# Optimization experiments

Measured on AMD Instinct MI355X. Metric: run time of the kernel, lower is better.

The kernel has to match this reference:

```python
import jax, jax.numpy as jnp
import numpy as np

HBLK = 16  # hadamard / nvfp4 block size
FP4_LEVELS = jnp.array([0.0, 0.5, 1.0, 1.5, 2.0, 3.0, 4.0, 6.0], dtype=jnp.float32)
FP4_MIDS = jnp.array([0.25, 0.75, 1.25, 1.75, 2.5, 3.5, 5.0], dtype=jnp.float32)


def _hadamard(n):
    H = np.array([[1.0]])
    while H.shape[0] < n:
        H = np.block([[H, H], [H, -H]])
    return jnp.asarray(H / np.sqrt(n), dtype=jnp.float32)  # orthonormal

H16 = _hadamard(HBLK)


def rht_forward(x, signs):
    # x: [M, K], K % 16 == 0 (no padding needed). Random sign diag then block Hadamard.
    M, K = x.shape
    xb = x.reshape(M, K // HBLK, HBLK)
    return ((xb * signs) @ H16).reshape(M, K)


def q_emulate(x):
    # NVFP4 quantize->dequantize along last dim: blocks of 16, E4M3 block scale = amax/6,
    # round-to-nearest onto E2M1 grid {0,.5,1,1.5,2,3,4,6} (signed).
    M, K = x.shape
    xb = x.reshape(M, K // HBLK, HBLK)
    amax = jnp.max(jnp.abs(xb), axis=-1, keepdims=True)
    scale = (amax / 6.0).astype(jnp.float8_e4m3fn).astype(x.dtype)
    safe = jnp.where(scale == 0, 1.0, scale)
    a = jnp.clip(jnp.abs(xb) / safe, 0.0, 6.0)
    q = FP4_LEVELS[jnp.searchsorted(FP4_MIDS, a)]
    return (jnp.sign(xb) * q * scale).reshape(M, K)


def setup_inputs() -> dict:
    key = jax.random.key(0)
    kx, kw, kb, ks1, ks2 = jax.random.split(key, 5)
    IN, OUT = 4096, 4096
    x = jax.random.normal(kx, (4, 2048, IN), dtype=jnp.float32)
    weight = jax.random.normal(kw, (OUT, IN), dtype=jnp.float32) / np.sqrt(IN)
    bound = 1.0 / np.sqrt(IN)
    bias = jax.random.uniform(kb, (OUT,), dtype=jnp.float32, minval=-bound, maxval=bound)
    signs_in = jnp.where(jax.random.bernoulli(ks1, 0.5, (HBLK,)), 1.0, -1.0).astype(jnp.float32)
    signs_grad = jnp.where(jax.random.bernoulli(ks2, 0.5, (HBLK,)), 1.0, -1.0).astype(jnp.float32)
    return {"x": x, "weight": weight, "bias": bias, "signs_in": signs_in, "signs_grad": signs_grad}


def reference(x, weight, bias, signs_in, signs_grad):
    # signs_grad only used in backward (kept for interface parity).
    x_flat = x.reshape(-1, x.shape[-1])
    x_q = q_emulate(rht_forward(x_flat, signs_in))
    w_q = q_emulate(rht_forward(weight, signs_in))
    y = x_q @ w_q.T + bias
    return y.reshape(*x.shape[:-1], weight.shape[0])
```

## Files before the change

kernel.cpp:

```cpp
#include <hip/hip_runtime.h>
#include <stdint.h>


typedef __bf16 bf16x8 __attribute__((ext_vector_type(8)));
typedef float f32x4 __attribute__((ext_vector_type(4)));


__device__ __forceinline__ float e4m3_rt(float x) {
    unsigned int u = __float_as_uint(x);
    int ex = (int)((u >> 23) & 0xffu) - 127;
    if (ex < -6) ex = -6;
    float qs = __uint_as_float((unsigned)(127 + 3 - ex) << 23);
    float qi = __uint_as_float((unsigned)(127 + ex - 3) << 23);
    return rintf(x * qs) * qi;
}

__global__ __launch_bounds__(256) void quant_rht_kernel(
    const float* __restrict__ X, const float* __restrict__ signs,
    uint16_t* __restrict__ Q, int ngroups)
{
    int gid = blockIdx.x * 256 + threadIdx.x;
    if (gid >= ngroups) return;

    const float4* p = (const float4*)(X + (size_t)gid * 16);
    float4 v0 = p[0], v1 = p[1], v2 = p[2], v3 = p[3];
    float t[16] = { v0.x, v0.y, v0.z, v0.w, v1.x, v1.y, v1.z, v1.w,
                    v2.x, v2.y, v2.z, v2.w, v3.x, v3.y, v3.z, v3.w };
#pragma unroll
    for (int i = 0; i < 16; i++) t[i] *= signs[i];

#pragma unroll
    for (int len = 1; len < 16; len <<= 1) {
#pragma unroll
        for (int i = 0; i < 16; i += 2 * len) {
#pragma unroll
            for (int j = 0; j < len; j++) {
                float a = t[i + j], b = t[i + j + len];
                t[i + j] = a + b;
                t[i + j + len] = a - b;
            }
        }
    }
    float amax = 0.0f;
#pragma unroll
    for (int i = 0; i < 16; i++) { t[i] *= 0.25f; amax = fmaxf(amax, fabsf(t[i])); }

    float scale = e4m3_rt(amax / 6.0f);
    float safe = (scale == 0.0f) ? 1.0f : scale;

    unsigned int w[8];
#pragma unroll
    for (int i = 0; i < 8; i++) {
        float d01[2];
#pragma unroll
        for (int h = 0; h < 2; h++) {
            float tv = t[2 * i + h];
            float aa = fminf(fabsf(tv) / safe, 6.0f);
            float q = aa > 2.5f ? (aa > 5.0f ? 6.0f : (aa > 3.5f ? 4.0f : 3.0f))
                                : (aa > 1.25f ? (aa > 1.75f ? 2.0f : 1.5f)
                                              : (aa > 0.75f ? 1.0f
                                                 : (aa > 0.25f ? 0.5f : 0.0f)));
            d01[h] = copysignf(q * scale, tv);
        }
        w[i] = (__float_as_uint(d01[0]) >> 16) |
               (__float_as_uint(d01[1]) & 0xFFFF0000u);
    }
    uint4* q4 = (uint4*)(Q + (size_t)gid * 16);
    q4[0] = make_uint4(w[0], w[1], w[2], w[3]);
    q4[1] = make_uint4(w[4], w[5], w[6], w[7]);
}


#define TM 128
#define TN 128
#define BK 64

__global__ __launch_bounds__(256) void gemm_bt_bias(
    const uint16_t* __restrict__ A,
    const uint16_t* __restrict__ B,
    const float* __restrict__ bias,
    float* __restrict__ C,
    int M, int N, int K)
{
    __shared__ uint4 As[TM * BK / 8];
    __shared__ uint4 Bs[TN * BK / 8];

    const int tid  = threadIdx.x;
    const int bm   = blockIdx.y, bn = blockIdx.x;
    const int wave = tid >> 6,  lane = tid & 63;
    const int wm   = wave >> 1, wn = wave & 1;
    const int lm   = lane & 15, g4 = lane >> 4;

    const int sr = tid >> 3;
    const int kg = (tid & 7) ^ (sr & 7);
    const uint16_t* ag = A + (size_t)(bm * TM + sr) * (size_t)K + kg * 8;
    const uint16_t* bg = B + (size_t)(bn * TN + sr) * (size_t)K + kg * 8;
    char* asd = (char*)&As[0] + tid * 16;
    char* bsd = (char*)&Bs[0] + tid * 16;

    f32x4 acc[4][4];
#pragma unroll
    for (int i = 0; i < 4; i++)
#pragma unroll
        for (int j = 0; j < 4; j++) acc[i][j] = (f32x4){0.f, 0.f, 0.f, 0.f};

    for (int kt = 0; kt < K; kt += BK) {
        __syncthreads();
#pragma unroll
        for (int i = 0; i < 4; i++) {
            __builtin_amdgcn_global_load_lds(
                (const __attribute__((address_space(1))) unsigned int*)(ag + (size_t)i * 32 * K),
                (__attribute__((address_space(3))) unsigned int*)(asd + i * 4096),
                16, 0, 0);
            __builtin_amdgcn_global_load_lds(
                (const __attribute__((address_space(1))) unsigned int*)(bg + (size_t)i * 32 * K),
                (__attribute__((address_space(3))) unsigned int*)(bsd + i * 4096),
                16, 0, 0);
        }
        ag += BK; bg += BK;
        __syncthreads();

#pragma unroll
        for (int ks = 0; ks < 2; ks++) {
            bf16x8 af[4], bf[4];
#pragma unroll
            for (int i = 0; i < 4; i++) {
                int rA = wm * 64 + i * 16 + lm;
                af[i] = __builtin_bit_cast(bf16x8, As[rA * 8 + ((ks * 4 + g4) ^ (lm & 7))]);
                int rB = wn * 64 + i * 16 + lm;
                bf[i] = __builtin_bit_cast(bf16x8, Bs[rB * 8 + ((ks * 4 + g4) ^ (lm & 7))]);
            }
#pragma unroll
            for (int i = 0; i < 4; i++)
#pragma unroll
                for (int j = 0; j < 4; j++)
                    acc[i][j] = __builtin_amdgcn_mfma_f32_16x16x32_bf16(
                        af[i], bf[j], acc[i][j], 0, 0, 0);
        }
    }

#pragma unroll
    for (int j = 0; j < 4; j++) {
        int col = bn * TN + wn * 64 + j * 16 + lm;
        float bj = bias[col];
#pragma unroll
        for (int i = 0; i < 4; i++) {
            int row0 = bm * TM + wm * 64 + i * 16 + g4 * 4;
#pragma unroll
            for (int r = 0; r < 4; r++) {
                C[(size_t)(row0 + r) * (size_t)N + col] = acc[i][j][r] + bj;
            }
        }
    }
}


extern "C" void kernel_launch(void* const* d_in, const int* in_sizes, int n_in,
                              void* d_out, int out_size, void* d_ws, size_t ws_size,
                              hipStream_t stream)
{
    const float* x        = (const float*)d_in[0];
    const float* w        = (const float*)d_in[1];
    const float* bias     = (const float*)d_in[2];
    const float* signs_in = (const float*)d_in[3];

    const int OUT = in_sizes[2];
    const int IN  = in_sizes[1] / OUT;
    const int M   = in_sizes[0] / IN;

    uint16_t* xq = (uint16_t*)d_ws;
    uint16_t* wq = xq + (size_t)M * (size_t)IN;
    (void)ws_size; (void)n_in; (void)out_size;

    int ngx = (int)((size_t)M * IN / 16);
    int ngw = (int)((size_t)OUT * IN / 16);
    quant_rht_kernel<<<(ngx + 255) / 256, 256, 0, stream>>>(x, signs_in, xq, ngx);
    quant_rht_kernel<<<(ngw + 255) / 256, 256, 0, stream>>>(w, signs_in, wq, ngw);

    dim3 grid(OUT / TN, M / TM);
    gemm_bt_bias<<<grid, 256, 0, stream>>>(xq, wq, bias, (float*)d_out, M, OUT, IN);
}
```

Baseline: 586.6 us.

## Rewrite GEMM as 256x256 multi-stage pipelined kernel and stage quant I/O via LDS

The GEMM moves from 128x128 tiles with 256 threads and a single LDS buffer to 256x256 tiles with 512 threads. It uses an 8-slot LDS ring of half-tiles filled by global_load_lds several stages ahead, with explicit vmcnt/lgkmcnt waits, barriers and setprio around the MFMA phases, so global loads overlap compute and reuse per tile increases. The quantize kernel now stages its input and output through swizzled shared memory so both reads and writes are coalesced. The bounds checks are dropped, so the code assumes the sizes divide evenly, and the deeper pipeline uses more LDS and registers.

```diff
diff --git a/kernel.cpp b/kernel.cpp
--- a/kernel.cpp
+++ b/kernel.cpp
@@ -19,15 +19,32 @@
     const float* __restrict__ X, const float* __restrict__ signs,
     uint16_t* __restrict__ Q, int ngroups)
 {
-    int gid = blockIdx.x * 256 + threadIdx.x;
-    if (gid >= ngroups) return;
-
-    const float4* p = (const float4*)(X + (size_t)gid * 16);
-    float4 v0 = p[0], v1 = p[1], v2 = p[2], v3 = p[3];
-    float t[16] = { v0.x, v0.y, v0.z, v0.w, v1.x, v1.y, v1.z, v1.w,
-                    v2.x, v2.y, v2.z, v2.w, v3.x, v3.y, v3.z, v3.w };
-#pragma unroll
-    for (int i = 0; i < 16; i++) t[i] *= signs[i];
+    (void)ngroups;
+    __shared__ uint4 sbuf[1024];
+    const int t = threadIdx.x;
+    const size_t gbase = (size_t)blockIdx.x * 256;
+
+    const uint4* src = (const uint4*)(X + gbase * 16);
+#pragma unroll
+    for (int it = 0; it < 4; ++it) {
+        int c = it * 256 + t;
+        sbuf[c ^ ((c >> 3) & 7)] = src[c];
+    }
+    __syncthreads();
+
+    float tv[16];
+#pragma unroll
+    for (int i = 0; i < 4; ++i) {
+        int c = 4 * t + i;
+        uint4 u = sbuf[c ^ ((c >> 3) & 7)];
+        tv[4 * i + 0] = __uint_as_float(u.x);
+        tv[4 * i + 1] = __uint_as_float(u.y);
+        tv[4 * i + 2] = __uint_as_float(u.z);
+        tv[4 * i + 3] = __uint_as_float(u.w);
+    }
+
+#pragma unroll
+    for (int i = 0; i < 16; i++) tv[i] *= signs[i];
 
 #pragma unroll
     for (int len = 1; len < 16; len <<= 1) {
@@ -35,15 +52,15 @@
         for (int i = 0; i < 16; i += 2 * len) {
 #pragma unroll
             for (int j = 0; j < len; j++) {
-                float a = t[i + j], b = t[i + j + len];
-                t[i + j] = a + b;
-                t[i + j + len] = a - b;
+                float a = tv[i + j], b = tv[i + j + len];
+                tv[i + j] = a + b;
+                tv[i + j + len] = a - b;
             }
         }
     }
     float amax = 0.0f;
 #pragma unroll
-    for (int i = 0; i < 16; i++) { t[i] *= 0.25f; amax = fmaxf(amax, fabsf(t[i])); }
+    for (int i = 0; i < 16; i++) { tv[i] *= 0.25f; amax = fmaxf(amax, fabsf(tv[i])); }
 
     float scale = e4m3_rt(amax / 6.0f);
     float safe = (scale == 0.0f) ? 1.0f : scale;
@@ -54,100 +71,159 @@
         float d01[2];
 #pragma unroll
         for (int h = 0; h < 2; h++) {
-            float tv = t[2 * i + h];
-            float aa = fminf(fabsf(tv) / safe, 6.0f);
+            float x = tv[2 * i + h];
+            float aa = fminf(fabsf(x) / safe, 6.0f);
             float q = aa > 2.5f ? (aa > 5.0f ? 6.0f : (aa > 3.5f ? 4.0f : 3.0f))
                                 : (aa > 1.25f ? (aa > 1.75f ? 2.0f : 1.5f)
                                               : (aa > 0.75f ? 1.0f
                                                  : (aa > 0.25f ? 0.5f : 0.0f)));
-            d01[h] = copysignf(q * scale, tv);
+            d01[h] = copysignf(q * scale, x);
         }
         w[i] = (__float_as_uint(d01[0]) >> 16) |
                (__float_as_uint(d01[1]) & 0xFFFF0000u);
     }
-    uint4* q4 = (uint4*)(Q + (size_t)gid * 16);
-    q4[0] = make_uint4(w[0], w[1], w[2], w[3]);
-    q4[1] = make_uint4(w[4], w[5], w[6], w[7]);
-}
-
-
-#define TM 128
-#define TN 128
-#define BK 64
-
-__global__ __launch_bounds__(256) void gemm_bt_bias(
+
+    __syncthreads();
+    {
+        int c0 = 2 * t, c1 = 2 * t + 1;
+        sbuf[c0 ^ ((c0 >> 3) & 7)] = make_uint4(w[0], w[1], w[2], w[3]);
+        sbuf[c1 ^ ((c1 >> 3) & 7)] = make_uint4(w[4], w[5], w[6], w[7]);
+    }
+    __syncthreads();
+
+    uint4* dst = (uint4*)(Q + gbase * 16);
+#pragma unroll
+    for (int it = 0; it < 2; ++it) {
+        int c = it * 256 + t;
+        dst[c] = sbuf[c ^ ((c >> 3) & 7)];
+    }
+}
+
+
+#define BM 256
+#define BN 256
+
+__global__ __launch_bounds__(512, 2) void gemm_bt_bias(
     const uint16_t* __restrict__ A,
     const uint16_t* __restrict__ B,
     const float* __restrict__ bias,
     float* __restrict__ C,
     int M, int N, int K)
 {
-    __shared__ uint4 As[TM * BK / 8];
-    __shared__ uint4 Bs[TN * BK / 8];
+    __shared__ uint4 sh[8][1024];
 
     const int tid  = threadIdx.x;
-    const int bm   = blockIdx.y, bn = blockIdx.x;
-    const int wave = tid >> 6,  lane = tid & 63;
-    const int wm   = wave >> 1, wn = wave & 1;
-    const int lm   = lane & 15, g4 = lane >> 4;
-
-    const int sr = tid >> 3;
-    const int kg = (tid & 7) ^ (sr & 7);
-    const uint16_t* ag = A + (size_t)(bm * TM + sr) * (size_t)K + kg * 8;
-    const uint16_t* bg = B + (size_t)(bn * TN + sr) * (size_t)K + kg * 8;
-    char* asd = (char*)&As[0] + tid * 16;
-    char* bsd = (char*)&Bs[0] + tid * 16;
-
-    f32x4 acc[4][4];
-#pragma unroll
-    for (int i = 0; i < 4; i++)
-#pragma unroll
-        for (int j = 0; j < 4; j++) acc[i][j] = (f32x4){0.f, 0.f, 0.f, 0.f};
-
-    for (int kt = 0; kt < K; kt += BK) {
-        __syncthreads();
-#pragma unroll
-        for (int i = 0; i < 4; i++) {
-            __builtin_amdgcn_global_load_lds(
-                (const __attribute__((address_space(1))) unsigned int*)(ag + (size_t)i * 32 * K),
-                (__attribute__((address_space(3))) unsigned int*)(asd + i * 4096),
-                16, 0, 0);
-            __builtin_amdgcn_global_load_lds(
-                (const __attribute__((address_space(1))) unsigned int*)(bg + (size_t)i * 32 * K),
-                (__attribute__((address_space(3))) unsigned int*)(bsd + i * 4096),
-                16, 0, 0);
-        }
-        ag += BK; bg += BK;
-        __syncthreads();
-
-#pragma unroll
-        for (int ks = 0; ks < 2; ks++) {
-            bf16x8 af[4], bf[4];
-#pragma unroll
-            for (int i = 0; i < 4; i++) {
-                int rA = wm * 64 + i * 16 + lm;
-                af[i] = __builtin_bit_cast(bf16x8, As[rA * 8 + ((ks * 4 + g4) ^ (lm & 7))]);
-                int rB = wn * 64 + i * 16 + lm;
-                bf[i] = __builtin_bit_cast(bf16x8, Bs[rB * 8 + ((ks * 4 + g4) ^ (lm & 7))]);
-            }
-#pragma unroll
-            for (int i = 0; i < 4; i++)
-#pragma unroll
-                for (int j = 0; j < 4; j++)
-                    acc[i][j] = __builtin_amdgcn_mfma_f32_16x16x32_bf16(
-                        af[i], bf[j], acc[i][j], 0, 0, 0);
-        }
-    }
-
-#pragma unroll
-    for (int j = 0; j < 4; j++) {
-        int col = bn * TN + wn * 64 + j * 16 + lm;
+    const int lane = tid & 63;
+    const int wave = tid >> 6;
+    const int wm = wave >> 2, wn = wave & 3;
+    const int lm = lane & 15, g4 = lane >> 4;
+    const int bn = blockIdx.x, bm = blockIdx.y;
+
+    const int NT  = K >> 6;
+    const int NHT = NT << 2;
+
+    const int p0 = tid, p1 = 512 + tid;
+    const int c0 = p0 ^ ((p0 >> 3) & 7);
+    const int c1 = p1 ^ ((p1 >> 3) & 7);
+    const uint16_t* asrc0 = A + (size_t)(bm * BM + (c0 >> 2)) * K + (c0 & 3) * 8;
+    const uint16_t* asrc1 = A + (size_t)(bm * BM + (c1 >> 2)) * K + (c1 & 3) * 8;
+    const uint16_t* bsrc0 = B + (size_t)(bn * BN + (c0 >> 2)) * K + (c0 & 3) * 8;
+    const uint16_t* bsrc1 = B + (size_t)(bn * BN + (c1 >> 2)) * K + (c1 & 3) * 8;
+    char* ldsd0 = (char*)&sh[0][0] + p0 * 16;
+    char* ldsd1 = (char*)&sh[0][0] + p1 * 16;
+
+    int aPos[8], bPos[4];
+#pragma unroll
+    for (int f = 0; f < 8; ++f) {
+        int c = (wm * 128 + f * 16 + lm) * 4 + g4;
+        aPos[f] = c ^ ((c >> 3) & 7);
+    }
+#pragma unroll
+    for (int f = 0; f < 4; ++f) {
+        int c = (wn * 64 + f * 16 + lm) * 4 + g4;
+        bPos[f] = c ^ ((c >> 3) & 7);
+    }
+
+    f32x4 acc[8][4];
+#pragma unroll
+    for (int i = 0; i < 8; ++i)
+#pragma unroll
+        for (int j = 0; j < 4; ++j) acc[i][j] = (f32x4){0.f, 0.f, 0.f, 0.f};
+    bf16x8 bfr[4];
+
+#define STAGE(jj) do {                                                        \
+    int _j = (jj);                                                            \
+    int _koff = (_j < NHT) ? (((_j >> 2) << 6) | (((_j >> 1) & 1) << 5)) : 0; \
+    int _sb = (_j & 7) << 14;                                                 \
+    const uint16_t* _s0 = (_j & 1) ? bsrc0 : asrc0;                           \
+    const uint16_t* _s1 = (_j & 1) ? bsrc1 : asrc1;                           \
+    __builtin_amdgcn_global_load_lds(                                         \
+        (const __attribute__((address_space(1))) unsigned int*)(_s0 + _koff), \
+        (__attribute__((address_space(3))) unsigned int*)(ldsd0 + _sb),       \
+        16, 0, 0);                                                            \
+    __builtin_amdgcn_global_load_lds(                                         \
+        (const __attribute__((address_space(1))) unsigned int*)(_s1 + _koff), \
+        (__attribute__((address_space(3))) unsigned int*)(ldsd1 + _sb),       \
+        16, 0, 0);                                                            \
+} while (0)
+
+#define PHASE(PAR, KS, RH, Q, GATE) do {                                      \
+    bf16x8 af_[4];                                                            \
+    _Pragma("unroll")                                                         \
+    for (int _i = 0; _i < 4; ++_i)                                            \
+        af_[_i] = __builtin_bit_cast(bf16x8,                                  \
+            sh[4*(PAR) + 2*(KS)][aPos[4*(RH) + _i]]);                         \
+    if ((Q) & 1) {                                                            \
+        _Pragma("unroll")                                                     \
+        for (int _jj = 0; _jj < 4; ++_jj)                                     \
+            bfr[_jj] = __builtin_bit_cast(bf16x8,                             \
+                sh[4*(PAR) + 2*(KS) + 1][bPos[_jj]]);                         \
+    }                                                                         \
+    STAGE(hb + 5 + (Q));                                                      \
+    __builtin_amdgcn_s_barrier();                                             \
+    asm volatile("s_waitcnt lgkmcnt(0)" ::: "memory");                        \
+    __builtin_amdgcn_s_setprio(1);                                            \
+    _Pragma("unroll")                                                         \
+    for (int _i = 0; _i < 4; ++_i)                                            \
+        _Pragma("unroll")                                                     \
+        for (int _jj = 0; _jj < 4; ++_jj)                                     \
+            acc[4*(RH) + _i][_jj] = __builtin_amdgcn_mfma_f32_16x16x32_bf16(  \
+                af_[_i], bfr[_jj], acc[4*(RH) + _i][_jj], 0, 0, 0);           \
+    __builtin_amdgcn_s_setprio(0);                                            \
+    if (GATE) asm volatile("s_waitcnt vmcnt(4)" ::: "memory");                \
+    __builtin_amdgcn_s_barrier();                                             \
+} while (0)
+
+    STAGE(0); STAGE(1); STAGE(2); STAGE(3); STAGE(4); STAGE(5);
+    asm volatile("s_waitcnt vmcnt(4)" ::: "memory");
+    __builtin_amdgcn_s_barrier();
+
+    const int NT2 = NT >> 1;
+    for (int it2 = 0; it2 < NT2; ++it2) {
+        const int hb = it2 << 3;
+        PHASE(0, 0, 0, 1, 0);
+        PHASE(0, 0, 1, 2, 0);
+        PHASE(0, 1, 0, 3, 0);
+        PHASE(0, 1, 1, 4, 1);
+        PHASE(1, 0, 0, 5, 0);
+        PHASE(1, 0, 1, 6, 0);
+        PHASE(1, 1, 0, 7, 0);
+        PHASE(1, 1, 1, 8, 1);
+    }
+    asm volatile("s_waitcnt vmcnt(0)" ::: "memory");
+
+#undef PHASE
+#undef STAGE
+
+#pragma unroll
+    for (int j = 0; j < 4; ++j) {
+        int col = bn * BN + wn * 64 + j * 16 + lm;
         float bj = bias[col];
 #pragma unroll
-        for (int i = 0; i < 4; i++) {
-            int row0 = bm * TM + wm * 64 + i * 16 + g4 * 4;
-#pragma unroll
-            for (int r = 0; r < 4; r++) {
+        for (int i = 0; i < 8; ++i) {
+            int row0 = bm * BM + wm * 128 + i * 16 + g4 * 4;
+#pragma unroll
+            for (int r = 0; r < 4; ++r) {
                 C[(size_t)(row0 + r) * (size_t)N + col] = acc[i][j][r] + bj;
             }
         }
@@ -174,9 +250,9 @@
 
     int ngx = (int)((size_t)M * IN / 16);
     int ngw = (int)((size_t)OUT * IN / 16);
-    quant_rht_kernel<<<(ngx + 255) / 256, 256, 0, stream>>>(x, signs_in, xq, ngx);
-    quant_rht_kernel<<<(ngw + 255) / 256, 256, 0, stream>>>(w, signs_in, wq, ngw);
-
-    dim3 grid(OUT / TN, M / TM);
-    gemm_bt_bias<<<grid, 256, 0, stream>>>(xq, wq, bias, (float*)d_out, M, OUT, IN);
-}
+    quant_rht_kernel<<<ngx / 256, 256, 0, stream>>>(x, signs_in, xq, ngx);
+    quant_rht_kernel<<<ngw / 256, 256, 0, stream>>>(w, signs_in, wq, ngw);
+
+    dim3 grid(OUT / BN, M / BM);
+    gemm_bt_bias<<<grid, 512, 0, stream>>>(xq, wq, bias, (float*)d_out, M, OUT, IN);
+}
```

After: 495.9 us. -15.5%, faster.
